# Optimization experiments

Hardware: AMD Instinct MI355X
Metric: run time of the kernel (lower is better)

The kernel has to match this reference:

```python
import jax, jax.numpy as jnp
import numpy as np

B, S, H, NH = 2, 2048, 768, 12
HD = H // NH  # 64


def setup_inputs() -> dict:
    key = jax.random.key(0)
    ks = jax.random.split(key, 4)
    scale = 1.0 / np.sqrt(H)
    return {
        "hidden_states": jax.random.normal(ks[0], (B, S, H), dtype=jnp.float32),
        "Wq": jax.random.normal(ks[1], (H, H), dtype=jnp.float32) * scale,
        "bq": jnp.zeros((H,), dtype=jnp.float32),
        "Wk": jax.random.normal(ks[2], (H, H), dtype=jnp.float32) * scale,
        "bk": jnp.zeros((H,), dtype=jnp.float32),
        "Wv": jax.random.normal(ks[3], (H, H), dtype=jnp.float32) * scale,
        "bv": jnp.zeros((H,), dtype=jnp.float32),
    }


def _split_heads(x):
    # [B,S,H] -> [B,NH,S,HD]  (transpose_for_scores)
    b, s, _ = x.shape
    return x.reshape(b, s, NH, HD).transpose(0, 2, 1, 3)


def reference(hidden_states, Wq, bq, Wk, bk, Wv, bv):
    q = _split_heads(hidden_states @ Wq + bq)  # [B,NH,S,HD]
    k = _split_heads(hidden_states @ Wk + bk)
    v = _split_heads(hidden_states @ Wv + bv)
    # delegated attn_fn(q,k,v): scaled-dot-product softmax attention
    scores = jnp.einsum("bhqd,bhkd->bhqk", q, k) / jnp.sqrt(jnp.asarray(HD, q.dtype))
    probs = jax.nn.softmax(scores, axis=-1)
    ctx = jnp.einsum("bhqk,bhkd->bhqd", probs, v)  # [B,NH,S,HD]
    # merge heads back: permute(0,2,1,3) then view to [B,S,H]
    out = ctx.transpose(0, 2, 1, 3).reshape(B, S, NH * HD)
    return out
```

## Files before the change

kernel.cpp:

```cpp
#include <hip/hip_runtime.h>
#include <stdint.h>

typedef __bf16 bf16_t;
typedef __bf16 bf16x8 __attribute__((ext_vector_type(8)));
typedef float f32x4 __attribute__((ext_vector_type(4)));
typedef float f32x16 __attribute__((ext_vector_type(16)));
typedef unsigned int u32x2 __attribute__((ext_vector_type(2)));

#define DEV __device__ __forceinline__

DEV void gload_lds16(const void* g, void* lds) {
  __builtin_amdgcn_global_load_lds(
      (const __attribute__((address_space(1))) uint32_t*)g,
      (__attribute__((address_space(3))) uint32_t*)lds, 16, 0, 0);
}

DEV float fexp2(float x) {
#if __has_builtin(__builtin_amdgcn_exp2f)
  return __builtin_amdgcn_exp2f(x);
#else
  return exp2f(x);
#endif
}

DEV uint32_t pk_bf16(float a, float b) {
  uint32_t lo = (uint32_t)__builtin_bit_cast(uint16_t, (bf16_t)a);
  uint32_t hi = (uint32_t)__builtin_bit_cast(uint16_t, (bf16_t)b);
  return lo | (hi << 16);
}

__global__ __launch_bounds__(256) void cvt_hs(const float* __restrict__ x,
                                              bf16_t* __restrict__ y) {
  int i = blockIdx.x * 256 + threadIdx.x;
  float4 v = ((const float4*)x)[i];
  ((uint2*)y)[i] = make_uint2(pk_bf16(v.x, v.y), pk_bf16(v.z, v.w));
}

__global__ __launch_bounds__(256) void cvt_w(const float* __restrict__ Wq,
                                             const float* __restrict__ Wk,
                                             const float* __restrict__ Wv,
                                             bf16_t* __restrict__ WT) {
  __shared__ float T[32][36];
  const int bx = blockIdx.x;
  const int by = blockIdx.y;
  const int p = bx / 24;
  const float* W = (p == 0) ? Wq : ((p == 1) ? Wk : Wv);
  const int n0 = bx * 32, nn0 = n0 - p * 768, k0 = by * 32;
  const int t = threadIdx.x;
  {
    int r = t >> 3, c4 = (t & 7) * 4;
    float4 v = *(const float4*)&W[(size_t)(k0 + r) * 768 + nn0 + c4];
    T[r][c4 + 0] = v.x; T[r][c4 + 1] = v.y; T[r][c4 + 2] = v.z; T[r][c4 + 3] = v.w;
  }
  __syncthreads();
  {
    int nr = t >> 3, kc = (t & 7) * 4;
    uint32_t lo = pk_bf16(T[kc + 0][nr], T[kc + 1][nr]);
    uint32_t hi = pk_bf16(T[kc + 2][nr], T[kc + 3][nr]);
    *(uint2*)&WT[(size_t)(n0 + nr) * 768 + k0 + kc] = make_uint2(lo, hi);
  }
}

__global__ __launch_bounds__(256) void gemm_qkv(
    const bf16_t* __restrict__ A, const bf16_t* __restrict__ Wt,
    const float* __restrict__ bq, const float* __restrict__ bk,
    const float* __restrict__ bv, bf16_t* __restrict__ Qo,
    bf16_t* __restrict__ Ko, bf16_t* __restrict__ VTo) {
  __shared__ __align__(16) char smem[65536];
  bf16_t* Cs = (bf16_t*)smem;
  const int bx = blockIdx.x;
  const int by = blockIdx.y;
  const int m0 = by * 128, n0 = bx * 128;
  const int tid = threadIdx.x, w = tid >> 6, lane = tid & 63;
  const int mw = (w & 1) * 64, nw = (w >> 1) * 64;
  const int quad = lane >> 4, col = lane & 15;

  f32x4 acc[4][4];
  for (int i = 0; i < 4; i++)
    for (int j = 0; j < 4; j++) acc[i][j] = (f32x4){0.f, 0.f, 0.f, 0.f};

  const int srow = w * 32 + (lane >> 3);
  const int scol = (lane & 7) * 8;
  const bf16_t* ag = A + (size_t)(m0 + srow) * 768 + scol;
  const bf16_t* bg = Wt + (size_t)(n0 + srow) * 768 + scol;

  auto stageg = [&](int kk, int bf) {
    const int k0 = kk * 64;
    bf16_t* dA = (bf16_t*)(smem + bf * 32768) + (w * 32) * 64;
    bf16_t* dB = (bf16_t*)(smem + bf * 32768 + 16384) + (w * 32) * 64;
#pragma unroll
    for (int i = 0; i < 4; i++) {
      gload_lds16(ag + (size_t)i * 8 * 768 + k0, dA + i * 8 * 64);
      gload_lds16(bg + (size_t)i * 8 * 768 + k0, dB + i * 8 * 64);
    }
  };

  stageg(0, 0);
  __syncthreads();

  for (int kk = 0; kk < 12; ++kk) {
    const int bf = kk & 1;
    if (kk < 11) stageg(kk + 1, bf ^ 1);
    __builtin_amdgcn_sched_barrier(0);
    const bf16_t* As = (const bf16_t*)(smem + bf * 32768);
    const bf16_t* Bs = (const bf16_t*)(smem + bf * 32768 + 16384);
#pragma unroll
    for (int ks = 0; ks < 2; ++ks) {
      bf16x8 af[4], bfr[4];
#pragma unroll
      for (int mt = 0; mt < 4; ++mt)
        af[mt] = *(const bf16x8*)&As[(mw + mt * 16 + col) * 64 + ks * 32 + quad * 8];
#pragma unroll
      for (int nt = 0; nt < 4; ++nt)
        bfr[nt] = *(const bf16x8*)&Bs[(nw + nt * 16 + col) * 64 + ks * 32 + quad * 8];
#pragma unroll
      for (int mt = 0; mt < 4; ++mt)
#pragma unroll
        for (int nt = 0; nt < 4; ++nt)
          acc[mt][nt] = __builtin_amdgcn_mfma_f32_16x16x32_bf16(
              af[mt], bfr[nt], acc[mt][nt], 0, 0, 0);
    }
    __syncthreads();
  }

  const int p = bx / 6;
  const float* bp = (p == 0) ? bq : ((p == 1) ? bk : bv);
  const float kscale = (p == 1) ? 0.18033688011112042f : 1.0f;
  const int bb0 = m0 >> 11, s0 = m0 & 2047;
  if (p < 2) {
#pragma unroll
    for (int nt = 0; nt < 4; nt++) {
      int n = nw + nt * 16 + col;
      float bias = bp[n0 + n - p * 768];
#pragma unroll
      for (int mt = 0; mt < 4; mt++)
#pragma unroll
        for (int r = 0; r < 4; r++) {
          int m = mw + mt * 16 + quad * 4 + r;
          Cs[m * 136 + n] = (bf16_t)((acc[mt][nt][r] + bias) * kscale);
        }
    }
    __syncthreads();
    bf16_t* dst = (p == 0) ? Qo : Ko;
#pragma unroll
    for (int i = 0; i < 8; i++) {
      int idx = i * 256 + tid;
      int m = idx >> 4, c = idx & 15;
      bf16x8 v = *(const bf16x8*)&Cs[m * 136 + c * 8];
      int nn = n0 - p * 768 + c * 8;
      int hq = nn >> 6, hd = nn & 63;
      *(bf16x8*)&dst[(size_t)((bb0 * 12 + hq) * 2048 + s0 + m) * 64 + hd] = v;
    }
  } else {
#pragma unroll
    for (int nt = 0; nt < 4; nt++) {
      int n = nw + nt * 16 + col;
      float bias = bp[n0 + n - 1536];
#pragma unroll
      for (int mt = 0; mt < 4; mt++)
#pragma unroll
        for (int r = 0; r < 4; r++) {
          int m = mw + mt * 16 + quad * 4 + r;
          Cs[n * 136 + m] = (bf16_t)(acc[mt][nt][r] + bias);
        }
    }
    __syncthreads();
#pragma unroll
    for (int i = 0; i < 8; i++) {
      int idx = i * 256 + tid;
      int n = idx >> 4, c = idx & 15;
      bf16x8 v = *(const bf16x8*)&Cs[n * 136 + c * 8];
      int nn = n0 - 1536 + n;
      int hq = nn >> 6, hd = nn & 63;
      *(bf16x8*)&VTo[((size_t)(bb0 * 12 + hq) * 64 + hd) * 2048 + s0 + c * 8] = v;
    }
  }
}

__global__ __launch_bounds__(256, 3) void attn(const bf16_t* __restrict__ Q,
                                               const bf16_t* __restrict__ K,
                                               const bf16_t* __restrict__ VT,
                                               float* __restrict__ Op,
                                               float* __restrict__ lp) {
  __shared__ __align__(16) char smem[49152];
  bf16_t* Kl = (bf16_t*)smem;
  bf16_t* Vl = (bf16_t*)(smem + 24576);
  const int id = blockIdx.x;
  const int rr0 = id >> 3;
  const int bh = (id & 7) * 3 + (rr0 >> 5);
  const int w5 = rr0 & 31;
  const int qt = w5 & 15, sp = w5 >> 4;
  const int tid = threadIdx.x, wv = tid >> 6, lane = tid & 63;
  const int lq = lane & 31, half = lane >> 5;
  const int q0 = qt * 128 + wv * 32;

  bf16x8 qf[4];
#pragma unroll
  for (int ks = 0; ks < 4; ++ks)
    qf[ks] = *(const bf16x8*)&Q[(size_t)(bh * 2048 + q0 + lq) * 64 + ks * 16 + half * 8];

  f32x16 oacc[2];
  for (int i = 0; i < 16; i++) { oacc[0][i] = 0.f; oacc[1][i] = 0.f; }
  float l0 = 0.f, l1 = 0.f, l2 = 0.f, l3 = 0.f;

  const bf16_t* gK = K + (size_t)bh * 2048 * 64 + (size_t)sp * 1024 * 64;
  const bf16_t* gV = VT + (size_t)bh * 64 * 2048 + sp * 1024;
  const int srow = lane >> 3, scc = lane & 7;
  const int cg = scc ^ srow;
  const bf16_t* gKb = gK + srow * 64 + cg * 8;
  const bf16_t* gVb = gV + srow * 2048 + cg * 8;
  const int kpart = (wv & 1) * 4;

  auto stage = [&](int kb, int buf) {
    if (wv < 2) {
#pragma unroll
      for (int i = 0; i < 4; i++) {
        int ii = kpart + i;
        gload_lds16(gKb + kb * 4096 + ii * 512, Kl + buf * 4096 + ii * 512);
      }
    } else {
#pragma unroll
      for (int i = 0; i < 4; i++) {
        int ii = kpart + i;
        gload_lds16(gVb + (size_t)ii * 16384 + kb * 64, Vl + buf * 4096 + ii * 512);
      }
    }
  };

  stage(0, 0);
  stage(1, 1);
  asm volatile("s_waitcnt vmcnt(4)" ::: "memory");
  __builtin_amdgcn_s_barrier();
  asm volatile("" ::: "memory");

  int bb = 0, rb = 2;
  for (int kb = 0; kb < 16; ++kb) {
    if (kb < 14) stage(kb + 2, rb);

    f32x16 sacc[2];
    for (int i = 0; i < 16; i++) { sacc[0][i] = 0.f; sacc[1][i] = 0.f; }
    __builtin_amdgcn_s_setprio(1);
#pragma unroll
    for (int t = 0; t < 2; t++) {
      const int row = t * 32 + lq;
#pragma unroll
      for (int ks = 0; ks < 4; ++ks) {
        bf16x8 kf = *(const bf16x8*)&Kl[bb * 4096 + row * 64 + (((2 * ks + half) ^ (row & 7)) * 8)];
        sacc[t] = __builtin_amdgcn_mfma_f32_32x32x16_bf16(kf, qf[ks], sacc[t], 0, 0, 0);
      }
    }
    __builtin_amdgcn_s_setprio(0);

#pragma unroll
    for (int t = 0; t < 2; t++)
#pragma unroll
      for (int rr = 0; rr < 16; rr++) sacc[t][rr] = fexp2(sacc[t][rr]);
#pragma unroll
    for (int rr = 0; rr < 16; rr += 4) {
      l0 += sacc[0][rr + 0] + sacc[1][rr + 0];
      l1 += sacc[0][rr + 1] + sacc[1][rr + 1];
      l2 += sacc[0][rr + 2] + sacc[1][rr + 2];
      l3 += sacc[0][rr + 3] + sacc[1][rr + 3];
    }

    uint32_t pkq[2][4][2];
#pragma unroll
    for (int t = 0; t < 2; t++)
#pragma unroll
      for (int g = 0; g < 4; g++) {
        pkq[t][g][0] = pk_bf16(sacc[t][4 * g + 0], sacc[t][4 * g + 1]);
        pkq[t][g][1] = pk_bf16(sacc[t][4 * g + 2], sacc[t][4 * g + 3]);
      }

    bf16x8 pfrag[4];
#pragma unroll
    for (int t = 0; t < 2; t++)
#pragma unroll
      for (int e = 0; e < 2; e++) {
        union { uint32_t u[4]; bf16x8 v; } F;
#pragma unroll
        for (int wd = 0; wd < 2; wd++) {
#if __has_builtin(__builtin_amdgcn_permlane32_swap)
          u32x2 sw = __builtin_amdgcn_permlane32_swap(pkq[t][2 * e][wd],
                                                      pkq[t][2 * e + 1][wd],
                                                      false, false);
          F.u[wd] = sw.x;
          F.u[2 + wd] = sw.y;
#else
          uint32_t s = half ? pkq[t][2 * e][wd] : pkq[t][2 * e + 1][wd];
          uint32_t rx = __shfl_xor(s, 32);
          uint32_t ow = half ? pkq[t][2 * e + 1][wd] : pkq[t][2 * e][wd];
          F.u[wd] = half ? rx : ow;
          F.u[2 + wd] = half ? ow : rx;
#endif
        }
        pfrag[2 * t + e] = F.v;
      }

    __builtin_amdgcn_s_setprio(1);
#pragma unroll
    for (int c = 0; c < 4; c++) {
#pragma unroll
      for (int dt = 0; dt < 2; dt++) {
        const int vr = dt * 32 + lq;
        bf16x8 vf = *(const bf16x8*)&Vl[bb * 4096 + vr * 64 + (((2 * c + half) ^ (vr & 7)) * 8)];
        oacc[dt] = __builtin_amdgcn_mfma_f32_32x32x16_bf16(vf, pfrag[c], oacc[dt], 0, 0, 0);
      }
    }
    __builtin_amdgcn_s_setprio(0);

    if (kb < 14) {
      asm volatile("s_waitcnt vmcnt(4)" ::: "memory");
    } else if (kb == 14) {
      asm volatile("s_waitcnt vmcnt(0)" ::: "memory");
    }
    if (kb < 15) {
      __builtin_amdgcn_s_barrier();
      asm volatile("" ::: "memory");
    }
    bb = (bb == 2) ? 0 : bb + 1;
    rb = (rb == 2) ? 0 : rb + 1;
  }

  float l_own = (l0 + l1) + (l2 + l3);
  float l_tot = l_own + __shfl_xor(l_own, 32);
  __syncthreads();
  float* Of = (float*)smem + wv * 2048;
#pragma unroll
  for (int dt = 0; dt < 2; dt++)
#pragma unroll
    for (int rr = 0; rr < 16; rr++) {
      int d = dt * 32 + (rr & 3) + 8 * (rr >> 2) + 4 * half;
      int g = d >> 2, wd = d & 3;
      Of[lq * 64 + ((g ^ (lq & 15)) * 4) + wd] = oacc[dt][rr];
    }
  if (half == 0) lp[((size_t)sp * 24 + bh) * 2048 + q0 + lq] = l_tot;
  float* ob = Op + (((size_t)sp * 24 + bh) * 2048 + q0) * 64;
#pragma unroll
  for (int i = 0; i < 8; i++) {
    int idx = i * 64 + lane;
    int qq = idx >> 4, c = idx & 15;
    f32x4 v = *(f32x4*)&Of[qq * 64 + ((c ^ (qq & 15)) * 4)];
    *(f32x4*)&ob[(size_t)qq * 64 + c * 4] = v;
  }
}

__global__ __launch_bounds__(256) void combine(const float* __restrict__ Op,
                                               const float* __restrict__ lp,
                                               float* __restrict__ out) {
  int g = blockIdx.x * 256 + threadIdx.x;
  int bh = g >> 15;
  int rem = g & 32767;
  int q = rem >> 4, c = rem & 15;
  const size_t plane = (size_t)24 * 2048 * 64;
  size_t o0 = ((size_t)bh * 2048 + q) * 64 + c * 4;
  f32x4 a = *(const f32x4*)&Op[o0];
  f32x4 b2 = *(const f32x4*)&Op[plane + o0];
  float l = lp[bh * 2048 + q] + lp[24 * 2048 + bh * 2048 + q];
  float inv = 1.0f / l;
  int b = bh / 12, head = bh % 12;
  f32x4 r;
#pragma unroll
  for (int j = 0; j < 4; j++) r[j] = (a[j] + b2[j]) * inv;
  *(f32x4*)&out[((size_t)b * 2048 + q) * 768 + head * 64 + c * 4] = r;
}

extern "C" void kernel_launch(void* const* d_in, const int* in_sizes, int n_in,
                              void* d_out, int out_size, void* d_ws, size_t ws_size,
                              hipStream_t stream) {
  const float* hs = (const float*)d_in[0];
  const float* Wq = (const float*)d_in[1];
  const float* bq = (const float*)d_in[2];
  const float* Wk = (const float*)d_in[3];
  const float* bk = (const float*)d_in[4];
  const float* Wv = (const float*)d_in[5];
  const float* bv = (const float*)d_in[6];
  float* out = (float*)d_out;

  char* w = (char*)d_ws;
  bf16_t* hsb = (bf16_t*)w; w += (size_t)4096 * 768 * 2;
  bf16_t* wtb = (bf16_t*)w; w += (size_t)2304 * 768 * 2;
  bf16_t* Qb  = (bf16_t*)w; w += (size_t)24 * 2048 * 64 * 2;
  bf16_t* Kb  = (bf16_t*)w; w += (size_t)24 * 2048 * 64 * 2;
  bf16_t* VTb = (bf16_t*)w; w += (size_t)24 * 2048 * 64 * 2;
  float* Opw  = (float*)w;  w += (size_t)2 * 24 * 2048 * 64 * 4;
  float* lpw  = (float*)w;

  hipLaunchKernelGGL(cvt_hs, dim3(3072), dim3(256), 0, stream, hs, hsb);
  hipLaunchKernelGGL(cvt_w, dim3(72, 24), dim3(256), 0, stream, Wq, Wk, Wv, wtb);
  hipLaunchKernelGGL(gemm_qkv, dim3(18, 32), dim3(256), 0, stream, hsb, wtb, bq,
                     bk, bv, Qb, Kb, VTb);
  hipLaunchKernelGGL(attn, dim3(768), dim3(256), 0, stream, Qb, Kb, VTb, Opw, lpw);
  hipLaunchKernelGGL(combine, dim3(3072), dim3(256), 0, stream, Opw, lpw, out);
}
```

Baseline: 147.8 us.

## Split attention keys four ways with 32-key tiles and halved LDS for occupancy

The attention kernel now splits each head's 2048 keys into four 512-key partitions instead of two, doubling the grid to 1536 blocks. It processes 32-key tiles per step and halves the LDS footprint, which allows launch bounds of 6 blocks per CU instead of 3. The V tile gets a new packed swizzled LDS layout, and the output-staging epilogue is done in two phases so it fits in the smaller shared buffer. The intent is more parallelism and occupancy to hide latency. The cost is twice the partial-output traffic written to global memory and reduced by the combine kernel, plus more barriers per unit of work.

```diff
diff --git a/kernel.cpp b/kernel.cpp
--- a/kernel.cpp
+++ b/kernel.cpp
@@ -177,18 +177,18 @@
   }
 }
 
-__global__ __launch_bounds__(256, 3) void attn(const bf16_t* __restrict__ Q,
+__global__ __launch_bounds__(256, 6) void attn(const bf16_t* __restrict__ Q,
                                                const bf16_t* __restrict__ K,
                                                const bf16_t* __restrict__ VT,
                                                float* __restrict__ Op,
                                                float* __restrict__ lp) {
-  __shared__ __align__(16) char smem[49152];
+  __shared__ __align__(16) char smem[24576];
   bf16_t* Kl = (bf16_t*)smem;
-  bf16_t* Vl = (bf16_t*)(smem + 24576);
+  bf16_t* Vl = (bf16_t*)(smem + 12288);
   const int id = blockIdx.x;
   const int rr0 = id >> 3;
-  const int bh = (id & 7) * 3 + (rr0 >> 5);
-  const int w5 = rr0 & 31;
+  const int bh = (id & 7) * 3 + (rr0 >> 6);
+  const int w5 = rr0 & 63;
   const int qt = w5 & 15, sp = w5 >> 4;
   const int tid = threadIdx.x, wv = tid >> 6, lane = tid & 63;
   const int lq = lane & 31, half = lane >> 5;
@@ -203,33 +203,41 @@
   for (int i = 0; i < 16; i++) { oacc[0][i] = 0.f; oacc[1][i] = 0.f; }
   float l0 = 0.f, l1 = 0.f, l2 = 0.f, l3 = 0.f;
 
-  const bf16_t* gK = K + (size_t)bh * 2048 * 64 + (size_t)sp * 1024 * 64;
-  const bf16_t* gV = VT + (size_t)bh * 64 * 2048 + sp * 1024;
-  const int srow = lane >> 3, scc = lane & 7;
-  const int cg = scc ^ srow;
-  const bf16_t* gKb = gK + srow * 64 + cg * 8;
-  const bf16_t* gVb = gV + srow * 2048 + cg * 8;
-  const int kpart = (wv & 1) * 4;
+  const bf16_t* gK = K + ((size_t)bh * 2048 + sp * 512) * 64;
+  const bf16_t* gV = VT + (size_t)bh * 64 * 2048 + sp * 512;
+  const int l8 = lane >> 3, l7 = lane & 7;
+
+  int iiA[2];
+  size_t soff[2];
+#pragma unroll
+  for (int i = 0; i < 2; i++) {
+    int ii = (wv & 1) * 2 + i;
+    iiA[i] = ii;
+    int rl = ii * 8 + l8;
+    int cs = l7 ^ (rl & 7);
+    if (wv < 2) {
+      soff[i] = (size_t)rl * 64 + cs * 8;
+    } else {
+      int d = rl * 2 + (cs >> 2), kc = cs & 3;
+      soff[i] = (size_t)d * 2048 + kc * 8;
+    }
+  }
 
   auto stage = [&](int kb, int buf) {
     if (wv < 2) {
 #pragma unroll
-      for (int i = 0; i < 4; i++) {
-        int ii = kpart + i;
-        gload_lds16(gKb + kb * 4096 + ii * 512, Kl + buf * 4096 + ii * 512);
-      }
+      for (int i = 0; i < 2; i++)
+        gload_lds16(gK + (size_t)kb * 2048 + soff[i], Kl + buf * 2048 + iiA[i] * 512);
     } else {
 #pragma unroll
-      for (int i = 0; i < 4; i++) {
-        int ii = kpart + i;
-        gload_lds16(gVb + (size_t)ii * 16384 + kb * 64, Vl + buf * 4096 + ii * 512);
-      }
+      for (int i = 0; i < 2; i++)
+        gload_lds16(gV + soff[i] + kb * 32, Vl + buf * 2048 + iiA[i] * 512);
     }
   };
 
   stage(0, 0);
   stage(1, 1);
-  asm volatile("s_waitcnt vmcnt(4)" ::: "memory");
+  asm volatile("s_waitcnt vmcnt(2)" ::: "memory");
   __builtin_amdgcn_s_barrier();
   asm volatile("" ::: "memory");
 
@@ -237,80 +245,72 @@
   for (int kb = 0; kb < 16; ++kb) {
     if (kb < 14) stage(kb + 2, rb);
 
-    f32x16 sacc[2];
-    for (int i = 0; i < 16; i++) { sacc[0][i] = 0.f; sacc[1][i] = 0.f; }
+    f32x16 sacc;
+    for (int i = 0; i < 16; i++) sacc[i] = 0.f;
     __builtin_amdgcn_s_setprio(1);
 #pragma unroll
-    for (int t = 0; t < 2; t++) {
-      const int row = t * 32 + lq;
-#pragma unroll
-      for (int ks = 0; ks < 4; ++ks) {
-        bf16x8 kf = *(const bf16x8*)&Kl[bb * 4096 + row * 64 + (((2 * ks + half) ^ (row & 7)) * 8)];
-        sacc[t] = __builtin_amdgcn_mfma_f32_32x32x16_bf16(kf, qf[ks], sacc[t], 0, 0, 0);
+    for (int ks = 0; ks < 4; ++ks) {
+      bf16x8 kf = *(const bf16x8*)&Kl[bb * 2048 + lq * 64 + (((2 * ks + half) ^ (lq & 7)) * 8)];
+      sacc = __builtin_amdgcn_mfma_f32_32x32x16_bf16(kf, qf[ks], sacc, 0, 0, 0);
+    }
+    __builtin_amdgcn_s_setprio(0);
+
+#pragma unroll
+    for (int rr = 0; rr < 16; rr++) sacc[rr] = fexp2(sacc[rr]);
+#pragma unroll
+    for (int rr = 0; rr < 16; rr += 4) {
+      l0 += sacc[rr + 0];
+      l1 += sacc[rr + 1];
+      l2 += sacc[rr + 2];
+      l3 += sacc[rr + 3];
+    }
+
+    uint32_t pkq[4][2];
+#pragma unroll
+    for (int g = 0; g < 4; g++) {
+      pkq[g][0] = pk_bf16(sacc[4 * g + 0], sacc[4 * g + 1]);
+      pkq[g][1] = pk_bf16(sacc[4 * g + 2], sacc[4 * g + 3]);
+    }
+
+    bf16x8 pfrag[2];
+#pragma unroll
+    for (int e = 0; e < 2; e++) {
+      union { uint32_t u[4]; bf16x8 v; } F;
+#pragma unroll
+      for (int wd = 0; wd < 2; wd++) {
+#if __has_builtin(__builtin_amdgcn_permlane32_swap)
+        u32x2 sw = __builtin_amdgcn_permlane32_swap(pkq[2 * e][wd],
+                                                    pkq[2 * e + 1][wd],
+                                                    false, false);
+        F.u[wd] = sw.x;
+        F.u[2 + wd] = sw.y;
+#else
+        uint32_t s = half ? pkq[2 * e][wd] : pkq[2 * e + 1][wd];
+        uint32_t rx = __shfl_xor(s, 32);
+        uint32_t ow = half ? pkq[2 * e + 1][wd] : pkq[2 * e][wd];
+        F.u[wd] = half ? rx : ow;
+        F.u[2 + wd] = half ? ow : rx;
+#endif
       }
-    }
-    __builtin_amdgcn_s_setprio(0);
-
-#pragma unroll
-    for (int t = 0; t < 2; t++)
-#pragma unroll
-      for (int rr = 0; rr < 16; rr++) sacc[t][rr] = fexp2(sacc[t][rr]);
-#pragma unroll
-    for (int rr = 0; rr < 16; rr += 4) {
-      l0 += sacc[0][rr + 0] + sacc[1][rr + 0];
-      l1 += sacc[0][rr + 1] + sacc[1][rr + 1];
-      l2 += sacc[0][rr + 2] + sacc[1][rr + 2];
-      l3 += sacc[0][rr + 3] + sacc[1][rr + 3];
-    }
-
-    uint32_t pkq[2][4][2];
-#pragma unroll
-    for (int t = 0; t < 2; t++)
-#pragma unroll
-      for (int g = 0; g < 4; g++) {
-        pkq[t][g][0] = pk_bf16(sacc[t][4 * g + 0], sacc[t][4 * g + 1]);
-        pkq[t][g][1] = pk_bf16(sacc[t][4 * g + 2], sacc[t][4 * g + 3]);
-      }
-
-    bf16x8 pfrag[4];
-#pragma unroll
-    for (int t = 0; t < 2; t++)
-#pragma unroll
-      for (int e = 0; e < 2; e++) {
-        union { uint32_t u[4]; bf16x8 v; } F;
-#pragma unroll
-        for (int wd = 0; wd < 2; wd++) {
-#if __has_builtin(__builtin_amdgcn_permlane32_swap)
-          u32x2 sw = __builtin_amdgcn_permlane32_swap(pkq[t][2 * e][wd],
-                                                      pkq[t][2 * e + 1][wd],
-                                                      false, false);
-          F.u[wd] = sw.x;
-          F.u[2 + wd] = sw.y;
-#else
-          uint32_t s = half ? pkq[t][2 * e][wd] : pkq[t][2 * e + 1][wd];
-          uint32_t rx = __shfl_xor(s, 32);
-          uint32_t ow = half ? pkq[t][2 * e + 1][wd] : pkq[t][2 * e][wd];
-          F.u[wd] = half ? rx : ow;
-          F.u[2 + wd] = half ? ow : rx;
-#endif
-        }
-        pfrag[2 * t + e] = F.v;
-      }
+      pfrag[e] = F.v;
+    }
 
     __builtin_amdgcn_s_setprio(1);
 #pragma unroll
-    for (int c = 0; c < 4; c++) {
+    for (int c = 0; c < 2; c++) {
 #pragma unroll
       for (int dt = 0; dt < 2; dt++) {
-        const int vr = dt * 32 + lq;
-        bf16x8 vf = *(const bf16x8*)&Vl[bb * 4096 + vr * 64 + (((2 * c + half) ^ (vr & 7)) * 8)];
+        const int d = dt * 32 + lq;
+        const int rp = d >> 1;
+        const int cp = (d & 1) * 4 + 2 * c + half;
+        bf16x8 vf = *(const bf16x8*)&Vl[bb * 2048 + rp * 64 + ((cp ^ (rp & 7)) * 8)];
         oacc[dt] = __builtin_amdgcn_mfma_f32_32x32x16_bf16(vf, pfrag[c], oacc[dt], 0, 0, 0);
       }
     }
     __builtin_amdgcn_s_setprio(0);
 
     if (kb < 14) {
-      asm volatile("s_waitcnt vmcnt(4)" ::: "memory");
+      asm volatile("s_waitcnt vmcnt(2)" ::: "memory");
     } else if (kb == 14) {
       asm volatile("s_waitcnt vmcnt(0)" ::: "memory");
     }
@@ -324,24 +324,30 @@
 
   float l_own = (l0 + l1) + (l2 + l3);
   float l_tot = l_own + __shfl_xor(l_own, 32);
-  __syncthreads();
-  float* Of = (float*)smem + wv * 2048;
-#pragma unroll
-  for (int dt = 0; dt < 2; dt++)
-#pragma unroll
-    for (int rr = 0; rr < 16; rr++) {
-      int d = dt * 32 + (rr & 3) + 8 * (rr >> 2) + 4 * half;
-      int g = d >> 2, wd = d & 3;
-      Of[lq * 64 + ((g ^ (lq & 15)) * 4) + wd] = oacc[dt][rr];
-    }
   if (half == 0) lp[((size_t)sp * 24 + bh) * 2048 + q0 + lq] = l_tot;
   float* ob = Op + (((size_t)sp * 24 + bh) * 2048 + q0) * 64;
-#pragma unroll
-  for (int i = 0; i < 8; i++) {
-    int idx = i * 64 + lane;
-    int qq = idx >> 4, c = idx & 15;
-    f32x4 v = *(f32x4*)&Of[qq * 64 + ((c ^ (qq & 15)) * 4)];
-    *(f32x4*)&ob[(size_t)qq * 64 + c * 4] = v;
+  __syncthreads();
+#pragma unroll
+  for (int ph = 0; ph < 2; ++ph) {
+    if (ph == 0 ? (wv < 3) : (wv == 3)) {
+      float* Of = (float*)smem + (ph == 0 ? wv : 0) * 2048;
+#pragma unroll
+      for (int dt = 0; dt < 2; dt++)
+#pragma unroll
+        for (int rr = 0; rr < 16; rr++) {
+          int d = dt * 32 + (rr & 3) + 8 * (rr >> 2) + 4 * half;
+          int g = d >> 2, wd = d & 3;
+          Of[lq * 64 + ((g ^ (lq & 15)) * 4) + wd] = oacc[dt][rr];
+        }
+#pragma unroll
+      for (int i = 0; i < 8; i++) {
+        int idx = i * 64 + lane;
+        int qq = idx >> 4, c = idx & 15;
+        f32x4 v = *(f32x4*)&Of[qq * 64 + ((c ^ (qq & 15)) * 4)];
+        *(f32x4*)&ob[(size_t)qq * 64 + c * 4] = v;
+      }
+    }
+    __syncthreads();
   }
 }
 
@@ -354,14 +360,20 @@
   int q = rem >> 4, c = rem & 15;
   const size_t plane = (size_t)24 * 2048 * 64;
   size_t o0 = ((size_t)bh * 2048 + q) * 64 + c * 4;
-  f32x4 a = *(const f32x4*)&Op[o0];
-  f32x4 b2 = *(const f32x4*)&Op[plane + o0];
-  float l = lp[bh * 2048 + q] + lp[24 * 2048 + bh * 2048 + q];
+  f32x4 s = (f32x4){0.f, 0.f, 0.f, 0.f};
+  float l = 0.f;
+#pragma unroll
+  for (int p = 0; p < 4; p++) {
+    f32x4 a = *(const f32x4*)&Op[p * plane + o0];
+    l += lp[((size_t)p * 24 + bh) * 2048 + q];
+#pragma unroll
+    for (int j = 0; j < 4; j++) s[j] += a[j];
+  }
   float inv = 1.0f / l;
   int b = bh / 12, head = bh % 12;
   f32x4 r;
 #pragma unroll
-  for (int j = 0; j < 4; j++) r[j] = (a[j] + b2[j]) * inv;
+  for (int j = 0; j < 4; j++) r[j] = s[j] * inv;
   *(f32x4*)&out[((size_t)b * 2048 + q) * 768 + head * 64 + c * 4] = r;
 }
 
@@ -383,13 +395,13 @@
   bf16_t* Qb  = (bf16_t*)w; w += (size_t)24 * 2048 * 64 * 2;
   bf16_t* Kb  = (bf16_t*)w; w += (size_t)24 * 2048 * 64 * 2;
   bf16_t* VTb = (bf16_t*)w; w += (size_t)24 * 2048 * 64 * 2;
-  float* Opw  = (float*)w;  w += (size_t)2 * 24 * 2048 * 64 * 4;
+  float* Opw  = (float*)w;  w += (size_t)4 * 24 * 2048 * 64 * 4;
   float* lpw  = (float*)w;
 
   hipLaunchKernelGGL(cvt_hs, dim3(3072), dim3(256), 0, stream, hs, hsb);
   hipLaunchKernelGGL(cvt_w, dim3(72, 24), dim3(256), 0, stream, Wq, Wk, Wv, wtb);
   hipLaunchKernelGGL(gemm_qkv, dim3(18, 32), dim3(256), 0, stream, hsb, wtb, bq,
                      bk, bv, Qb, Kb, VTb);
-  hipLaunchKernelGGL(attn, dim3(768), dim3(256), 0, stream, Qb, Kb, VTb, Opw, lpw);
+  hipLaunchKernelGGL(attn, dim3(1536), dim3(256), 0, stream, Qb, Kb, VTb, Opw, lpw);
   hipLaunchKernelGGL(combine, dim3(3072), dim3(256), 0, stream, Opw, lpw, out);
 }
```

After: 196.0 us. +32.6%, slower.

## Load K/V fragments straight from global into registers, dropping LDS staging

Applied to the files above, without the earlier changes.

The attention kernel no longer stages K and V tiles through shared memory with async global-to-LDS loads and block barriers. Each wave now loads its own K and V^T MFMA fragments directly from global memory into registers, 32 keys per step, double-buffered in two register sets (A/B) with sched barriers between them. This removes LDS traffic and all per-iteration barriers, but every wave re-reads K/V from global/L2 instead of sharing one tile across four waves. It also raises register pressure, and its per-lane strided 16-byte loads may coalesce poorly.

```diff
diff --git a/kernel.cpp b/kernel.cpp
--- a/kernel.cpp
+++ b/kernel.cpp
@@ -182,9 +182,7 @@
                                                const bf16_t* __restrict__ VT,
                                                float* __restrict__ Op,
                                                float* __restrict__ lp) {
-  __shared__ __align__(16) char smem[49152];
-  bf16_t* Kl = (bf16_t*)smem;
-  bf16_t* Vl = (bf16_t*)(smem + 24576);
+  __shared__ float Of[4][2048];
   const int id = blockIdx.x;
   const int rr0 = id >> 3;
   const int bh = (id & 7) * 3 + (rr0 >> 5);
@@ -194,153 +192,113 @@
   const int lq = lane & 31, half = lane >> 5;
   const int q0 = qt * 128 + wv * 32;
 
-  bf16x8 qf[4];
-#pragma unroll
-  for (int ks = 0; ks < 4; ++ks)
-    qf[ks] = *(const bf16x8*)&Q[(size_t)(bh * 2048 + q0 + lq) * 64 + ks * 16 + half * 8];
+  bf16x8 qf0, qf1, qf2, qf3;
+  {
+    const bf16_t* qp = Q + (size_t)(bh * 2048 + q0 + lq) * 64 + half * 8;
+    qf0 = *(const bf16x8*)(qp + 0);
+    qf1 = *(const bf16x8*)(qp + 16);
+    qf2 = *(const bf16x8*)(qp + 32);
+    qf3 = *(const bf16x8*)(qp + 48);
+  }
 
   f32x16 oacc[2];
   for (int i = 0; i < 16; i++) { oacc[0][i] = 0.f; oacc[1][i] = 0.f; }
   float l0 = 0.f, l1 = 0.f, l2 = 0.f, l3 = 0.f;
 
-  const bf16_t* gK = K + (size_t)bh * 2048 * 64 + (size_t)sp * 1024 * 64;
-  const bf16_t* gV = VT + (size_t)bh * 64 * 2048 + sp * 1024;
-  const int srow = lane >> 3, scc = lane & 7;
-  const int cg = scc ^ srow;
-  const bf16_t* gKb = gK + srow * 64 + cg * 8;
-  const bf16_t* gVb = gV + srow * 2048 + cg * 8;
-  const int kpart = (wv & 1) * 4;
-
-  auto stage = [&](int kb, int buf) {
-    if (wv < 2) {
-#pragma unroll
-      for (int i = 0; i < 4; i++) {
-        int ii = kpart + i;
-        gload_lds16(gKb + kb * 4096 + ii * 512, Kl + buf * 4096 + ii * 512);
-      }
-    } else {
-#pragma unroll
-      for (int i = 0; i < 4; i++) {
-        int ii = kpart + i;
-        gload_lds16(gVb + (size_t)ii * 16384 + kb * 64, Vl + buf * 4096 + ii * 512);
-      }
-    }
-  };
-
-  stage(0, 0);
-  stage(1, 1);
-  asm volatile("s_waitcnt vmcnt(4)" ::: "memory");
-  __builtin_amdgcn_s_barrier();
-  asm volatile("" ::: "memory");
-
-  int bb = 0, rb = 2;
-  for (int kb = 0; kb < 16; ++kb) {
-    if (kb < 14) stage(kb + 2, rb);
-
-    f32x16 sacc[2];
-    for (int i = 0; i < 16; i++) { sacc[0][i] = 0.f; sacc[1][i] = 0.f; }
-    __builtin_amdgcn_s_setprio(1);
-#pragma unroll
-    for (int t = 0; t < 2; t++) {
-      const int row = t * 32 + lq;
-#pragma unroll
-      for (int ks = 0; ks < 4; ++ks) {
-        bf16x8 kf = *(const bf16x8*)&Kl[bb * 4096 + row * 64 + (((2 * ks + half) ^ (row & 7)) * 8)];
-        sacc[t] = __builtin_amdgcn_mfma_f32_32x32x16_bf16(kf, qf[ks], sacc[t], 0, 0, 0);
-      }
-    }
-    __builtin_amdgcn_s_setprio(0);
-
-#pragma unroll
-    for (int t = 0; t < 2; t++)
-#pragma unroll
-      for (int rr = 0; rr < 16; rr++) sacc[t][rr] = fexp2(sacc[t][rr]);
-#pragma unroll
-    for (int rr = 0; rr < 16; rr += 4) {
-      l0 += sacc[0][rr + 0] + sacc[1][rr + 0];
-      l1 += sacc[0][rr + 1] + sacc[1][rr + 1];
-      l2 += sacc[0][rr + 2] + sacc[1][rr + 2];
-      l3 += sacc[0][rr + 3] + sacc[1][rr + 3];
-    }
-
-    uint32_t pkq[2][4][2];
-#pragma unroll
-    for (int t = 0; t < 2; t++)
-#pragma unroll
-      for (int g = 0; g < 4; g++) {
-        pkq[t][g][0] = pk_bf16(sacc[t][4 * g + 0], sacc[t][4 * g + 1]);
-        pkq[t][g][1] = pk_bf16(sacc[t][4 * g + 2], sacc[t][4 * g + 3]);
-      }
-
-    bf16x8 pfrag[4];
-#pragma unroll
-    for (int t = 0; t < 2; t++)
-#pragma unroll
-      for (int e = 0; e < 2; e++) {
-        union { uint32_t u[4]; bf16x8 v; } F;
-#pragma unroll
-        for (int wd = 0; wd < 2; wd++) {
+  const bf16_t* kp = K + ((size_t)bh * 2048 + sp * 1024 + lq) * 64 + half * 8;
+  const bf16_t* vp = VT + (size_t)bh * 131072 + (size_t)lq * 2048 + sp * 1024 + half * 8;
+
+#define LOADKV(S, kbv)                                                \
+  S##k0 = *(const bf16x8*)(kp + (size_t)(kbv) * 2048 + 0);            \
+  S##k1 = *(const bf16x8*)(kp + (size_t)(kbv) * 2048 + 16);           \
+  S##k2 = *(const bf16x8*)(kp + (size_t)(kbv) * 2048 + 32);           \
+  S##k3 = *(const bf16x8*)(kp + (size_t)(kbv) * 2048 + 48);           \
+  S##v00 = *(const bf16x8*)(vp + (kbv) * 32 + 0);                     \
+  S##v01 = *(const bf16x8*)(vp + (kbv) * 32 + 16);                    \
+  S##v10 = *(const bf16x8*)(vp + 65536 + (kbv) * 32 + 0);             \
+  S##v11 = *(const bf16x8*)(vp + 65536 + (kbv) * 32 + 16);
+
 #if __has_builtin(__builtin_amdgcn_permlane32_swap)
-          u32x2 sw = __builtin_amdgcn_permlane32_swap(pkq[t][2 * e][wd],
-                                                      pkq[t][2 * e + 1][wd],
-                                                      false, false);
-          F.u[wd] = sw.x;
-          F.u[2 + wd] = sw.y;
+#define XHALF(a, b, F, wd)                                   \
+  { u32x2 sw_ = __builtin_amdgcn_permlane32_swap(a, b, false, false); \
+    F.u[wd] = sw_.x; F.u[2 + wd] = sw_.y; }
 #else
-          uint32_t s = half ? pkq[t][2 * e][wd] : pkq[t][2 * e + 1][wd];
-          uint32_t rx = __shfl_xor(s, 32);
-          uint32_t ow = half ? pkq[t][2 * e + 1][wd] : pkq[t][2 * e][wd];
-          F.u[wd] = half ? rx : ow;
-          F.u[2 + wd] = half ? ow : rx;
+#define XHALF(a, b, F, wd)                                   \
+  { uint32_t s_ = half ? (a) : (b);                          \
+    uint32_t rx_ = __shfl_xor(s_, 32);                       \
+    uint32_t ow_ = half ? (b) : (a);                         \
+    F.u[wd] = half ? rx_ : ow_; F.u[2 + wd] = half ? ow_ : rx_; }
 #endif
-        }
-        pfrag[2 * t + e] = F.v;
-      }
-
-    __builtin_amdgcn_s_setprio(1);
-#pragma unroll
-    for (int c = 0; c < 4; c++) {
-#pragma unroll
-      for (int dt = 0; dt < 2; dt++) {
-        const int vr = dt * 32 + lq;
-        bf16x8 vf = *(const bf16x8*)&Vl[bb * 4096 + vr * 64 + (((2 * c + half) ^ (vr & 7)) * 8)];
-        oacc[dt] = __builtin_amdgcn_mfma_f32_32x32x16_bf16(vf, pfrag[c], oacc[dt], 0, 0, 0);
-      }
-    }
-    __builtin_amdgcn_s_setprio(0);
-
-    if (kb < 14) {
-      asm volatile("s_waitcnt vmcnt(4)" ::: "memory");
-    } else if (kb == 14) {
-      asm volatile("s_waitcnt vmcnt(0)" ::: "memory");
-    }
-    if (kb < 15) {
-      __builtin_amdgcn_s_barrier();
-      asm volatile("" ::: "memory");
-    }
-    bb = (bb == 2) ? 0 : bb + 1;
-    rb = (rb == 2) ? 0 : rb + 1;
-  }
+
+#define COMPUTE(S)                                                          \
+  {                                                                         \
+    f32x16 sacc;                                                            \
+    for (int i_ = 0; i_ < 16; i_++) sacc[i_] = 0.f;                         \
+    __builtin_amdgcn_s_setprio(1);                                          \
+    sacc = __builtin_amdgcn_mfma_f32_32x32x16_bf16(S##k0, qf0, sacc, 0, 0, 0); \
+    sacc = __builtin_amdgcn_mfma_f32_32x32x16_bf16(S##k1, qf1, sacc, 0, 0, 0); \
+    sacc = __builtin_amdgcn_mfma_f32_32x32x16_bf16(S##k2, qf2, sacc, 0, 0, 0); \
+    sacc = __builtin_amdgcn_mfma_f32_32x32x16_bf16(S##k3, qf3, sacc, 0, 0, 0); \
+    __builtin_amdgcn_s_setprio(0);                                          \
+    _Pragma("unroll")                                                       \
+    for (int rr_ = 0; rr_ < 16; rr_++) sacc[rr_] = fexp2(sacc[rr_]);        \
+    _Pragma("unroll")                                                       \
+    for (int rr_ = 0; rr_ < 16; rr_ += 4) {                                 \
+      l0 += sacc[rr_ + 0]; l1 += sacc[rr_ + 1];                             \
+      l2 += sacc[rr_ + 2]; l3 += sacc[rr_ + 3];                             \
+    }                                                                       \
+    uint32_t q00 = pk_bf16(sacc[0], sacc[1]), q01 = pk_bf16(sacc[2], sacc[3]);   \
+    uint32_t q10 = pk_bf16(sacc[4], sacc[5]), q11 = pk_bf16(sacc[6], sacc[7]);   \
+    uint32_t q20 = pk_bf16(sacc[8], sacc[9]), q21 = pk_bf16(sacc[10], sacc[11]); \
+    uint32_t q30 = pk_bf16(sacc[12], sacc[13]), q31 = pk_bf16(sacc[14], sacc[15]); \
+    union { uint32_t u[4]; bf16x8 v; } F0, F1;                              \
+    XHALF(q00, q10, F0, 0); XHALF(q01, q11, F0, 1);                         \
+    XHALF(q20, q30, F1, 0); XHALF(q21, q31, F1, 1);                         \
+    __builtin_amdgcn_s_setprio(1);                                          \
+    oacc[0] = __builtin_amdgcn_mfma_f32_32x32x16_bf16(S##v00, F0.v, oacc[0], 0, 0, 0); \
+    oacc[1] = __builtin_amdgcn_mfma_f32_32x32x16_bf16(S##v10, F0.v, oacc[1], 0, 0, 0); \
+    oacc[0] = __builtin_amdgcn_mfma_f32_32x32x16_bf16(S##v01, F1.v, oacc[0], 0, 0, 0); \
+    oacc[1] = __builtin_amdgcn_mfma_f32_32x32x16_bf16(S##v11, F1.v, oacc[1], 0, 0, 0); \
+    __builtin_amdgcn_s_setprio(0);                                          \
+  }
+
+  bf16x8 Ak0, Ak1, Ak2, Ak3, Av00, Av01, Av10, Av11;
+  bf16x8 Bk0, Bk1, Bk2, Bk3, Bv00, Bv01, Bv10, Bv11;
+
+  LOADKV(A, 0);
+  LOADKV(B, 1);
+
+  for (int kb = 0; kb < 32; kb += 2) {
+    COMPUTE(A);
+    if (kb + 2 < 32) { LOADKV(A, kb + 2); }
+    __builtin_amdgcn_sched_barrier(0);
+    COMPUTE(B);
+    if (kb + 3 < 32) { LOADKV(B, kb + 3); }
+    __builtin_amdgcn_sched_barrier(0);
+  }
+
+#undef LOADKV
+#undef XHALF
+#undef COMPUTE
 
   float l_own = (l0 + l1) + (l2 + l3);
   float l_tot = l_own + __shfl_xor(l_own, 32);
-  __syncthreads();
-  float* Of = (float*)smem + wv * 2048;
+  if (half == 0) lp[((size_t)sp * 24 + bh) * 2048 + q0 + lq] = l_tot;
+  float* Ow = &Of[wv][0];
 #pragma unroll
   for (int dt = 0; dt < 2; dt++)
 #pragma unroll
     for (int rr = 0; rr < 16; rr++) {
       int d = dt * 32 + (rr & 3) + 8 * (rr >> 2) + 4 * half;
       int g = d >> 2, wd = d & 3;
-      Of[lq * 64 + ((g ^ (lq & 15)) * 4) + wd] = oacc[dt][rr];
-    }
-  if (half == 0) lp[((size_t)sp * 24 + bh) * 2048 + q0 + lq] = l_tot;
+      Ow[lq * 64 + ((g ^ (lq & 15)) * 4) + wd] = oacc[dt][rr];
+    }
   float* ob = Op + (((size_t)sp * 24 + bh) * 2048 + q0) * 64;
 #pragma unroll
   for (int i = 0; i < 8; i++) {
     int idx = i * 64 + lane;
     int qq = idx >> 4, c = idx & 15;
-    f32x4 v = *(f32x4*)&Of[qq * 64 + ((c ^ (qq & 15)) * 4)];
+    f32x4 v = *(f32x4*)&Ow[qq * 64 + ((c ^ (qq & 15)) * 4)];
     *(f32x4*)&ob[(size_t)qq * 64 + c * 4] = v;
   }
 }
```

Result: slower. 212.2 us (+43.6%).

## Software-pipeline QK^T of next key block with softmax and PV of current

Applied to the files above, without the earlier changes.

Restructures the attention loop so that the QK^T MFMAs for key block k+1 are issued before the exp, row-sum and PV work of block k. Two ping-pong score accumulators and a three-buffer rotation across LDS slots make this possible, and the loop is unrolled by two. The goal is to hide the exp and permlane work behind matrix-core work within one wave. In exchange it holds two score tiles in registers, which raises VGPR pressure. The prefetch wait also changes from vmcnt(4) to vmcnt(0) each step, which may expose more load latency.

```diff
diff --git a/kernel.cpp b/kernel.cpp
--- a/kernel.cpp
+++ b/kernel.cpp
@@ -227,104 +227,117 @@
     }
   };
 
+  f32x16 sA[2], sB[2];
+
+#if __has_builtin(__builtin_amdgcn_permlane32_swap)
+#define XHALF(a, b, F, wd)                                              \
+  { u32x2 sw_ = __builtin_amdgcn_permlane32_swap(a, b, false, false);   \
+    F.u[wd] = sw_.x; F.u[2 + wd] = sw_.y; }
+#else
+#define XHALF(a, b, F, wd)                                              \
+  { uint32_t s_ = half ? (a) : (b);                                     \
+    uint32_t rx_ = __shfl_xor(s_, 32);                                  \
+    uint32_t ow_ = half ? (b) : (a);                                    \
+    F.u[wd] = half ? rx_ : ow_; F.u[2 + wd] = half ? ow_ : rx_; }
+#endif
+
+#define QK(bt, S)                                                           \
+  {                                                                         \
+    for (int i_ = 0; i_ < 16; i_++) { S[0][i_] = 0.f; S[1][i_] = 0.f; }     \
+    __builtin_amdgcn_s_setprio(1);                                          \
+    _Pragma("unroll")                                                       \
+    for (int t_ = 0; t_ < 2; t_++) {                                        \
+      const int row_ = t_ * 32 + lq;                                        \
+      _Pragma("unroll")                                                     \
+      for (int ks_ = 0; ks_ < 4; ++ks_) {                                   \
+        bf16x8 kf_ = *(const bf16x8*)&Kl[(bt) * 4096 + row_ * 64 +          \
+                                         (((2 * ks_ + half) ^ (row_ & 7)) * 8)]; \
+        S[t_] = __builtin_amdgcn_mfma_f32_32x32x16_bf16(kf_, qf[ks_], S[t_], 0, 0, 0); \
+      }                                                                     \
+    }                                                                       \
+    __builtin_amdgcn_s_setprio(0);                                          \
+  }
+
+#define SMPV(bt, S)                                                         \
+  {                                                                         \
+    _Pragma("unroll")                                                       \
+    for (int t_ = 0; t_ < 2; t_++)                                          \
+      _Pragma("unroll")                                                     \
+      for (int rr_ = 0; rr_ < 16; rr_++) S[t_][rr_] = fexp2(S[t_][rr_]);    \
+    _Pragma("unroll")                                                       \
+    for (int rr_ = 0; rr_ < 16; rr_ += 4) {                                 \
+      l0 += S[0][rr_ + 0] + S[1][rr_ + 0];                                  \
+      l1 += S[0][rr_ + 1] + S[1][rr_ + 1];                                  \
+      l2 += S[0][rr_ + 2] + S[1][rr_ + 2];                                  \
+      l3 += S[0][rr_ + 3] + S[1][rr_ + 3];                                  \
+    }                                                                       \
+    uint32_t pkq_[2][4][2];                                                 \
+    _Pragma("unroll")                                                       \
+    for (int t_ = 0; t_ < 2; t_++)                                          \
+      _Pragma("unroll")                                                     \
+      for (int g_ = 0; g_ < 4; g_++) {                                      \
+        pkq_[t_][g_][0] = pk_bf16(S[t_][4 * g_ + 0], S[t_][4 * g_ + 1]);    \
+        pkq_[t_][g_][1] = pk_bf16(S[t_][4 * g_ + 2], S[t_][4 * g_ + 3]);    \
+      }                                                                     \
+    bf16x8 pfrag_[4];                                                       \
+    _Pragma("unroll")                                                       \
+    for (int t_ = 0; t_ < 2; t_++)                                          \
+      _Pragma("unroll")                                                     \
+      for (int e_ = 0; e_ < 2; e_++) {                                      \
+        union { uint32_t u[4]; bf16x8 v; } F;                               \
+        XHALF(pkq_[t_][2 * e_][0], pkq_[t_][2 * e_ + 1][0], F, 0);          \
+        XHALF(pkq_[t_][2 * e_][1], pkq_[t_][2 * e_ + 1][1], F, 1);          \
+        pfrag_[2 * t_ + e_] = F.v;                                          \
+      }                                                                     \
+    __builtin_amdgcn_s_setprio(1);                                          \
+    _Pragma("unroll")                                                       \
+    for (int c_ = 0; c_ < 4; c_++) {                                        \
+      _Pragma("unroll")                                                     \
+      for (int dt_ = 0; dt_ < 2; dt_++) {                                   \
+        const int vr_ = dt_ * 32 + lq;                                      \
+        bf16x8 vf_ = *(const bf16x8*)&Vl[(bt) * 4096 + vr_ * 64 +           \
+                                         (((2 * c_ + half) ^ (vr_ & 7)) * 8)]; \
+        oacc[dt_] = __builtin_amdgcn_mfma_f32_32x32x16_bf16(vf_, pfrag_[c_], oacc[dt_], 0, 0, 0); \
+      }                                                                     \
+    }                                                                       \
+    __builtin_amdgcn_s_setprio(0);                                          \
+  }
+
   stage(0, 0);
   stage(1, 1);
   asm volatile("s_waitcnt vmcnt(4)" ::: "memory");
   __builtin_amdgcn_s_barrier();
   asm volatile("" ::: "memory");
-
-  int bb = 0, rb = 2;
-  for (int kb = 0; kb < 16; ++kb) {
-    if (kb < 14) stage(kb + 2, rb);
-
-    f32x16 sacc[2];
-    for (int i = 0; i < 16; i++) { sacc[0][i] = 0.f; sacc[1][i] = 0.f; }
-    __builtin_amdgcn_s_setprio(1);
-#pragma unroll
-    for (int t = 0; t < 2; t++) {
-      const int row = t * 32 + lq;
-#pragma unroll
-      for (int ks = 0; ks < 4; ++ks) {
-        bf16x8 kf = *(const bf16x8*)&Kl[bb * 4096 + row * 64 + (((2 * ks + half) ^ (row & 7)) * 8)];
-        sacc[t] = __builtin_amdgcn_mfma_f32_32x32x16_bf16(kf, qf[ks], sacc[t], 0, 0, 0);
-      }
-    }
-    __builtin_amdgcn_s_setprio(0);
-
-#pragma unroll
-    for (int t = 0; t < 2; t++)
-#pragma unroll
-      for (int rr = 0; rr < 16; rr++) sacc[t][rr] = fexp2(sacc[t][rr]);
-#pragma unroll
-    for (int rr = 0; rr < 16; rr += 4) {
-      l0 += sacc[0][rr + 0] + sacc[1][rr + 0];
-      l1 += sacc[0][rr + 1] + sacc[1][rr + 1];
-      l2 += sacc[0][rr + 2] + sacc[1][rr + 2];
-      l3 += sacc[0][rr + 3] + sacc[1][rr + 3];
-    }
-
-    uint32_t pkq[2][4][2];
-#pragma unroll
-    for (int t = 0; t < 2; t++)
-#pragma unroll
-      for (int g = 0; g < 4; g++) {
-        pkq[t][g][0] = pk_bf16(sacc[t][4 * g + 0], sacc[t][4 * g + 1]);
-        pkq[t][g][1] = pk_bf16(sacc[t][4 * g + 2], sacc[t][4 * g + 3]);
-      }
-
-    bf16x8 pfrag[4];
-#pragma unroll
-    for (int t = 0; t < 2; t++)
-#pragma unroll
-      for (int e = 0; e < 2; e++) {
-        union { uint32_t u[4]; bf16x8 v; } F;
-#pragma unroll
-        for (int wd = 0; wd < 2; wd++) {
-#if __has_builtin(__builtin_amdgcn_permlane32_swap)
-          u32x2 sw = __builtin_amdgcn_permlane32_swap(pkq[t][2 * e][wd],
-                                                      pkq[t][2 * e + 1][wd],
-                                                      false, false);
-          F.u[wd] = sw.x;
-          F.u[2 + wd] = sw.y;
-#else
-          uint32_t s = half ? pkq[t][2 * e][wd] : pkq[t][2 * e + 1][wd];
-          uint32_t rx = __shfl_xor(s, 32);
-          uint32_t ow = half ? pkq[t][2 * e + 1][wd] : pkq[t][2 * e][wd];
-          F.u[wd] = half ? rx : ow;
-          F.u[2 + wd] = half ? ow : rx;
-#endif
-        }
-        pfrag[2 * t + e] = F.v;
-      }
-
-    __builtin_amdgcn_s_setprio(1);
-#pragma unroll
-    for (int c = 0; c < 4; c++) {
-#pragma unroll
-      for (int dt = 0; dt < 2; dt++) {
-        const int vr = dt * 32 + lq;
-        bf16x8 vf = *(const bf16x8*)&Vl[bb * 4096 + vr * 64 + (((2 * c + half) ^ (vr & 7)) * 8)];
-        oacc[dt] = __builtin_amdgcn_mfma_f32_32x32x16_bf16(vf, pfrag[c], oacc[dt], 0, 0, 0);
-      }
-    }
-    __builtin_amdgcn_s_setprio(0);
-
-    if (kb < 14) {
-      asm volatile("s_waitcnt vmcnt(4)" ::: "memory");
-    } else if (kb == 14) {
-      asm volatile("s_waitcnt vmcnt(0)" ::: "memory");
-    }
-    if (kb < 15) {
-      __builtin_amdgcn_s_barrier();
-      asm volatile("" ::: "memory");
-    }
-    bb = (bb == 2) ? 0 : bb + 1;
-    rb = (rb == 2) ? 0 : rb + 1;
-  }
+  QK(0, sA);
+  asm volatile("s_waitcnt vmcnt(0)" ::: "memory");
+  __builtin_amdgcn_s_barrier();
+  asm volatile("" ::: "memory");
+
+  int b_pv = 0, b_qk = 1, b_st = 2;
+  for (int kb = 0; kb < 16; kb += 2) {
+    if (kb < 14) stage(kb + 2, b_st);
+    if (kb < 15) QK(b_qk, sB);
+    SMPV(b_pv, sA);
+    asm volatile("s_waitcnt vmcnt(0)" ::: "memory");
+    __builtin_amdgcn_s_barrier();
+    asm volatile("" ::: "memory");
+    b_pv = b_qk; b_qk = b_st; b_st = (b_st == 2) ? 0 : b_st + 1;
+    if (kb + 1 < 14) stage(kb + 3, b_st);
+    if (kb + 1 < 15) QK(b_qk, sA);
+    SMPV(b_pv, sB);
+    asm volatile("s_waitcnt vmcnt(0)" ::: "memory");
+    __builtin_amdgcn_s_barrier();
+    asm volatile("" ::: "memory");
+    b_pv = b_qk; b_qk = b_st; b_st = (b_st == 2) ? 0 : b_st + 1;
+  }
+
+#undef QK
+#undef SMPV
+#undef XHALF
 
   float l_own = (l0 + l1) + (l2 + l3);
   float l_tot = l_own + __shfl_xor(l_own, 32);
-  __syncthreads();
+  if (half == 0) lp[((size_t)sp * 24 + bh) * 2048 + q0 + lq] = l_tot;
   float* Of = (float*)smem + wv * 2048;
 #pragma unroll
   for (int dt = 0; dt < 2; dt++)
@@ -334,7 +347,6 @@
       int g = d >> 2, wd = d & 3;
       Of[lq * 64 + ((g ^ (lq & 15)) * 4) + wd] = oacc[dt][rr];
     }
-  if (half == 0) lp[((size_t)sp * 24 + bh) * 2048 + q0 + lq] = l_tot;
   float* ob = Op + (((size_t)sp * 24 + bh) * 2048 + q0) * 64;
 #pragma unroll
   for (int i = 0; i < 8; i++) {
```

Result: slower. 182.3 us (+23.3%).
